# Kernel optimization log

Hardware: AMD Instinct MI355X
Metric: run time of the kernel (lower is better)

## Reference

```python
import jax, jax.numpy as jnp
import numpy as np

D_MODEL = 1024
NUM_HEADS = 16
D_K = D_MODEL // NUM_HEADS
LOCAL_WINDOW = 3
STRIDE = 4


def strided_mask(seq_len):
    # position i attends to j iff j <= i and (i-j <= local_window or (i-j) % stride == 0)
    i = jnp.arange(seq_len)[:, None]
    j = jnp.arange(seq_len)[None, :]
    d = i - j
    return (d >= 0) & ((d <= LOCAL_WINDOW) | (d % STRIDE == 0))


def setup_inputs() -> dict:
    key = jax.random.key(0)
    ks = jax.random.split(key, 11)
    B, S, D = 4, 1024, D_MODEL
    s = 1.0 / np.sqrt(D)
    inp = {
        "Q": jax.random.normal(ks[0], (B, S, D), jnp.float32),
        "K": jax.random.normal(ks[1], (B, S, D), jnp.float32),
        "V": jax.random.normal(ks[2], (B, S, D), jnp.float32),
        "Wq": jax.random.normal(ks[3], (D, D), jnp.float32) * s,
        "bq": jnp.zeros((D,), jnp.float32),
        "Wk": jax.random.normal(ks[4], (D, D), jnp.float32) * s,
        "bk": jnp.zeros((D,), jnp.float32),
        "Wv": jax.random.normal(ks[5], (D, D), jnp.float32) * s,
        "bv": jnp.zeros((D,), jnp.float32),
        "Wo": jax.random.normal(ks[6], (D, D), jnp.float32) * s,
        "bo": jnp.zeros((D,), jnp.float32),
    }
    return inp


def reference(Q, K, V, Wq, bq, Wk, bk, Wv, bv, Wo, bo):
    B, S, D = Q.shape
    H, dk = NUM_HEADS, D_K

    def split(x):  # [B,S,D] -> [B,H,S,dk]
        return x.reshape(B, S, H, dk).transpose(0, 2, 1, 3)

    q = split(Q @ Wq + bq)
    k = split(K @ Wk + bk)
    v = split(V @ Wv + bv)

    scores = jnp.einsum("bhsd,bhtd->bhst", q, k) / jnp.sqrt(
        jnp.asarray(dk, jnp.float32))
    m = strided_mask(S)[None, None]  # [1,1,S,S]
    scores = jnp.where(m, scores, -1e9)
    attn = jax.nn.softmax(scores, axis=-1)
    out = jnp.einsum("bhst,bhtd->bhsd", attn, v)
    out = out.transpose(0, 2, 1, 3).reshape(B, S, D)  # combine heads
    return out @ Wo + bo
```

## Files before the change

kernel.cpp:

```cpp
#include <hip/hip_runtime.h>

typedef _Float16 f16;
typedef __attribute__((ext_vector_type(8))) _Float16 f16x8;
typedef __attribute__((ext_vector_type(4))) _Float16 f16x4;
typedef __attribute__((ext_vector_type(4))) float f32x4;

#define MFMA16(a, b, c) __builtin_amdgcn_mfma_f32_16x16x32_f16((a), (b), (c), 0, 0, 0)

__device__ __forceinline__ void gld_lds16(const void* g, void* l) {
  __builtin_amdgcn_global_load_lds(
      (__attribute__((address_space(1))) void*)const_cast<void*>(g),
      (__attribute__((address_space(3))) void*)l, 16, 0, 0);
}

__device__ __forceinline__ f16x8 ld8(const f16* p) { return *(const f16x8*)p; }

__device__ __forceinline__ f16x8 cvt8(const float4& a, const float4& b) {
  f16x8 h;
  h[0] = (f16)a.x; h[1] = (f16)a.y; h[2] = (f16)a.z; h[3] = (f16)a.w;
  h[4] = (f16)b.x; h[5] = (f16)b.y; h[6] = (f16)b.z; h[7] = (f16)b.w;
  return h;
}

__global__ __launch_bounds__(256) void cvt_wT_kernel(
    const float* __restrict__ Wq, const float* __restrict__ Wk,
    const float* __restrict__ Wv, const float* __restrict__ Wo,
    f16* __restrict__ Tq, f16* __restrict__ Tk, f16* __restrict__ Tv, f16* __restrict__ To) {
  const int z = blockIdx.z;
  const float* W = z == 0 ? Wq : (z == 1 ? Wk : (z == 2 ? Wv : Wo));
  f16* T = z == 0 ? Tq : (z == 1 ? Tk : (z == 2 ? Tv : To));
  __shared__ float tile[64][65];
  const int k0 = blockIdx.x * 64, n0 = blockIdx.y * 64;
  const int tx = threadIdx.x & 63, ty = threadIdx.x >> 6;
#pragma unroll
  for (int rr = 0; rr < 16; ++rr) {
    int r = rr * 4 + ty;
    tile[r][tx] = W[(size_t)(k0 + r) * 1024 + n0 + tx];
  }
  __syncthreads();
#pragma unroll
  for (int rr = 0; rr < 16; ++rr) {
    int nn = rr * 4 + ty;
    T[(size_t)(n0 + nn) * 1024 + k0 + tx] = (f16)tile[tx][nn];
  }
}

__global__ __launch_bounds__(256) void gemm_qkv_kernel(
    const float* __restrict__ Q32, const float* __restrict__ K32, const float* __restrict__ V32,
    const f16* __restrict__ Bq, const f16* __restrict__ Bk, const f16* __restrict__ Bv,
    const float* __restrict__ bq, const float* __restrict__ bk, const float* __restrict__ bv,
    f16* __restrict__ qh, f16* __restrict__ kh, f16* __restrict__ kg,
    f16* __restrict__ vh, f16* __restrict__ vtg) {
  const int z = blockIdx.z;
  const float* A32 = z == 0 ? Q32 : (z == 1 ? K32 : V32);
  const f16* Bt = z == 0 ? Bq : (z == 1 ? Bk : Bv);
  const float* bias = z == 0 ? bq : (z == 1 ? bk : bv);

  __shared__ alignas(16) f16 lA[128 * 32];
  __shared__ alignas(16) f16 lB[128 * 32];

  const int t = threadIdx.x;
  const int w = t >> 6, lane = t & 63, quad = lane >> 4, l15 = lane & 15;
  const int wm = w >> 1, wn = w & 1;
  const int mbase = blockIdx.x * 128;
  const int nbase = blockIdx.y * 128;

  const f32x4 zero4 = {0.f, 0.f, 0.f, 0.f};
  f32x4 acc[4][4];
#pragma unroll
  for (int mi = 0; mi < 4; ++mi)
#pragma unroll
    for (int ni = 0; ni < 4; ++ni) acc[mi][ni] = zero4;

  const int r = t >> 2;
  const int koff = (t & 3) * 8;
  const float* ap0 = A32 + (size_t)(mbase + r) * 1024 + koff;
  const float* ap1 = A32 + (size_t)(mbase + 64 + r) * 1024 + koff;

  float4 pa0 = *(const float4*)(ap0);
  float4 pa1 = *(const float4*)(ap0 + 4);
  float4 pb0 = *(const float4*)(ap1);
  float4 pb1 = *(const float4*)(ap1 + 4);

  for (int k0 = 0; k0 < 1024; k0 += 32) {
    __syncthreads();
    *(f16x8*)((char*)lA + t * 16) = cvt8(pa0, pa1);
    *(f16x8*)((char*)lA + 4096 + t * 16) = cvt8(pb0, pb1);
    gld_lds16(Bt + (size_t)(nbase + r) * 1024 + k0 + koff, (char*)lB + w * 1024);
    gld_lds16(Bt + (size_t)(nbase + 64 + r) * 1024 + k0 + koff, (char*)lB + 4096 + w * 1024);
    if (k0 + 32 < 1024) {
      pa0 = *(const float4*)(ap0 + k0 + 32);
      pa1 = *(const float4*)(ap0 + k0 + 36);
      pb0 = *(const float4*)(ap1 + k0 + 32);
      pb1 = *(const float4*)(ap1 + k0 + 36);
    }
    __syncthreads();

    f16x8 af[4], bf[4];
#pragma unroll
    for (int mi = 0; mi < 4; ++mi)
      af[mi] = ld8(&lA[(wm * 64 + mi * 16 + l15) * 32 + quad * 8]);
#pragma unroll
    for (int ni = 0; ni < 4; ++ni)
      bf[ni] = ld8(&lB[(wn * 64 + ni * 16 + l15) * 32 + quad * 8]);
#pragma unroll
    for (int mi = 0; mi < 4; ++mi)
#pragma unroll
      for (int ni = 0; ni < 4; ++ni)
        acc[mi][ni] = MFMA16(af[mi], bf[ni], acc[mi][ni]);
  }

#pragma unroll
  for (int mi = 0; mi < 4; ++mi) {
#pragma unroll
    for (int ni = 0; ni < 4; ++ni) {
#pragma unroll
      for (int rg = 0; rg < 4; ++rg) {
        const int row = mbase + wm * 64 + mi * 16 + quad * 4 + rg;
        const int col = nbase + wn * 64 + ni * 16 + l15;
        const float v = acc[mi][ni][rg] + bias[col];
        const int bh = (row >> 10) * 16 + (col >> 6);
        const int s = row & 1023, d = col & 63;
        const f16 hv = (f16)v;
        if (z == 0) {
          qh[(size_t)bh * 65536 + s * 64 + d] = hv;
        } else if (z == 1) {
          kh[(size_t)bh * 65536 + s * 64 + d] = hv;
          kg[(((size_t)bh * 4 + (s & 3)) * 256 + (s >> 2)) * 64 + d] = hv;
        } else {
          vh[(size_t)bh * 65536 + s * 64 + d] = hv;
          const int rr = s & 3, n = s >> 2, wi = n & 63;
          vtg[(size_t)bh * 65536 + (size_t)rr * 16384 + (size_t)d * 256 +
              (n & ~63) + ((wi & 15) << 2) + (wi >> 4)] = hv;
        }
      }
    }
  }
}

__global__ __launch_bounds__(256) void gemm_out_kernel(
    const f16* __restrict__ A, const f16* __restrict__ Bt,
    const float* __restrict__ bias, float* __restrict__ Cf) {
  __shared__ alignas(16) f16 lA[64 * 32];
  __shared__ alignas(16) f16 lB[128 * 32];

  const int t = threadIdx.x;
  const int w = t >> 6, lane = t & 63, quad = lane >> 4, l15 = lane & 15;
  const int wm = w >> 1, wn = w & 1;
  const int mbase = blockIdx.x * 64;
  const int nbase = blockIdx.y * 128;

  const f32x4 zero4 = {0.f, 0.f, 0.f, 0.f};
  f32x4 acc[2][4];
#pragma unroll
  for (int mi = 0; mi < 2; ++mi)
#pragma unroll
    for (int ni = 0; ni < 4; ++ni) acc[mi][ni] = zero4;

  const int r = t >> 2;
  const int koff = (t & 3) * 8;

  for (int k0 = 0; k0 < 1024; k0 += 32) {
    __syncthreads();
    gld_lds16(A + (size_t)(mbase + r) * 1024 + k0 + koff, (char*)lA + w * 1024);
    gld_lds16(Bt + (size_t)(nbase + r) * 1024 + k0 + koff, (char*)lB + w * 1024);
    gld_lds16(Bt + (size_t)(nbase + 64 + r) * 1024 + k0 + koff, (char*)lB + 4096 + w * 1024);
    __syncthreads();

    f16x8 af[2], bf[4];
#pragma unroll
    for (int mi = 0; mi < 2; ++mi)
      af[mi] = ld8(&lA[(wm * 32 + mi * 16 + l15) * 32 + quad * 8]);
#pragma unroll
    for (int ni = 0; ni < 4; ++ni)
      bf[ni] = ld8(&lB[(wn * 64 + ni * 16 + l15) * 32 + quad * 8]);
#pragma unroll
    for (int mi = 0; mi < 2; ++mi)
#pragma unroll
      for (int ni = 0; ni < 4; ++ni)
        acc[mi][ni] = MFMA16(af[mi], bf[ni], acc[mi][ni]);
  }

#pragma unroll
  for (int mi = 0; mi < 2; ++mi)
#pragma unroll
    for (int ni = 0; ni < 4; ++ni)
#pragma unroll
      for (int rg = 0; rg < 4; ++rg) {
        const int row = mbase + wm * 32 + mi * 16 + quad * 4 + rg;
        const int col = nbase + wn * 64 + ni * 16 + l15;
        Cf[(size_t)row * 1024 + col] = acc[mi][ni][rg] + bias[col];
      }
}

__global__ __launch_bounds__(256) void attn_far_kernel(
    const f16* __restrict__ qh, const f16* __restrict__ kg,
    const f16* __restrict__ vtg, float* __restrict__ po, float* __restrict__ ml) {
  const int t = threadIdx.x;
  const int w = t >> 6, lane = t & 63, quad = lane >> 4, l15 = lane & 15;
  const int widx = blockIdx.x + 512 * w;
  const int bh = (widx & 255) >> 2, r = widx & 3;
  const int wq = widx >> 8;
  const int m0 = wq * 32;
  const int ntiles = (wq >> 1) + 1;

  __shared__ alignas(16) f16 lp[4][2][16 * 72];

  const f16* qb = qh + (size_t)bh * 65536;
  const f16* kb = kg + ((size_t)bh * 4 + r) * 16384;
  const f16* vb = vtg + (size_t)bh * 65536 + (size_t)r * 16384;
  const float SCL2 = 0.125f * 1.44269504f;

  f16x8 aq[2][2];
#pragma unroll
  for (int mt = 0; mt < 2; ++mt) {
    const int i = 4 * (m0 + mt * 16 + l15) + r;
#pragma unroll
    for (int ko = 0; ko < 2; ++ko)
      aq[mt][ko] = ld8(qb + (size_t)i * 64 + ko * 32 + quad * 8);
  }

  const f32x4 zero4 = {0.f, 0.f, 0.f, 0.f};
  f32x4 o[2][4];
  float mrun[2][4], lrun[2][4];
#pragma unroll
  for (int mt = 0; mt < 2; ++mt)
#pragma unroll
    for (int i = 0; i < 4; ++i) {
      o[mt][i] = zero4; mrun[mt][i] = -1e30f; lrun[mt][i] = 0.f;
    }

  for (int jt = 0; jt < ntiles; ++jt) {
    const int n0 = jt * 64;
    f16x8 bk0[4], bk1[4], bv0[4], bv1[4];
#pragma unroll
    for (int nt = 0; nt < 4; ++nt) {
      const f16* kr = kb + (size_t)(n0 + nt * 16 + l15) * 64;
      bk0[nt] = ld8(kr + quad * 8);
      bk1[nt] = ld8(kr + 32 + quad * 8);
      const f16* vr = vb + (size_t)(nt * 16 + l15) * 256 + n0;
      bv0[nt] = ld8(vr + quad * 8);
      bv1[nt] = ld8(vr + 32 + quad * 8);
    }
    const bool lastt = (jt == ntiles - 1);
#pragma unroll
    for (int mt = 0; mt < 2; ++mt) {
      f32x4 sc[4];
#pragma unroll
      for (int nt = 0; nt < 4; ++nt) {
        f32x4 c = MFMA16(aq[mt][0], bk0[nt], zero4);
        sc[nt] = MFMA16(aq[mt][1], bk1[nt], c);
      }
#pragma unroll
      for (int rg = 0; rg < 4; ++rg) {
        const int m = m0 + mt * 16 + quad * 4 + rg;
        float s[4];
#pragma unroll
        for (int nt = 0; nt < 4; ++nt) {
          float vsc = sc[nt][rg] * SCL2;
          if (lastt) vsc = (n0 + nt * 16 + l15 < m) ? vsc : -3.0e38f;
          s[nt] = vsc;
        }
        float tm = fmaxf(fmaxf(s[0], s[1]), fmaxf(s[2], s[3]));
        tm = fmaxf(tm, __shfl_xor(tm, 1));
        tm = fmaxf(tm, __shfl_xor(tm, 2));
        tm = fmaxf(tm, __shfl_xor(tm, 4));
        tm = fmaxf(tm, __shfl_xor(tm, 8));
        const float mnew = fmaxf(mrun[mt][rg], tm);
        const float alpha = exp2f(mrun[mt][rg] - mnew);
        float p[4], ps = 0.f;
#pragma unroll
        for (int nt = 0; nt < 4; ++nt) { p[nt] = exp2f(s[nt] - mnew); ps += p[nt]; }
        ps += __shfl_xor(ps, 1);
        ps += __shfl_xor(ps, 2);
        ps += __shfl_xor(ps, 4);
        ps += __shfl_xor(ps, 8);
        lrun[mt][rg] = lrun[mt][rg] * alpha + ps;
        mrun[mt][rg] = mnew;
#pragma unroll
        for (int ntv = 0; ntv < 4; ++ntv) o[mt][ntv][rg] *= alpha;
        f16x4 pk;
        pk.x = (f16)p[0]; pk.y = (f16)p[1]; pk.z = (f16)p[2]; pk.w = (f16)p[3];
        *(f16x4*)&lp[w][mt][(quad * 4 + rg) * 72 + l15 * 4] = pk;
      }
    }
#pragma unroll
    for (int mt = 0; mt < 2; ++mt) {
      const f16x8 ap0 = ld8(&lp[w][mt][l15 * 72 + quad * 8]);
      const f16x8 ap1 = ld8(&lp[w][mt][l15 * 72 + 32 + quad * 8]);
#pragma unroll
      for (int ntv = 0; ntv < 4; ++ntv) {
        f32x4 c = MFMA16(ap0, bv0[ntv], o[mt][ntv]);
        o[mt][ntv] = MFMA16(ap1, bv1[ntv], c);
      }
    }
  }

#pragma unroll
  for (int mt = 0; mt < 2; ++mt)
#pragma unroll
    for (int rg = 0; rg < 4; ++rg) {
      const int i = 4 * (m0 + mt * 16 + quad * 4 + rg) + r;
      const size_t idx = (size_t)bh * 1024 + i;
#pragma unroll
      for (int ntv = 0; ntv < 4; ++ntv)
        po[idx * 64 + ntv * 16 + l15] = o[mt][ntv][rg];
      if (l15 == 0) { ml[idx * 2] = mrun[mt][rg]; ml[idx * 2 + 1] = lrun[mt][rg]; }
    }
}

__global__ __launch_bounds__(256) void attn_diag_kernel(
    const f16* __restrict__ qh, const f16* __restrict__ kh, const f16* __restrict__ vh,
    const float* __restrict__ po, const float* __restrict__ ml, f16* __restrict__ ao) {
  const int t = threadIdx.x;
  const int widx = blockIdx.x * 4 + (t >> 6);
  const int l = t & 63;
  const int bh = widx >> 10, i = widx & 1023;
  const float SCL2 = 0.125f * 1.44269504f;

  const float q = (float)qh[(size_t)bh * 65536 + (size_t)i * 64 + l];
  float s[4];
#pragma unroll
  for (int d = 0; d < 4; ++d) {
    const int j = i - d;
    const int jc = j < 0 ? 0 : j;
    float pr = q * (float)kh[(size_t)bh * 65536 + (size_t)jc * 64 + l];
    pr += __shfl_xor(pr, 1);
    pr += __shfl_xor(pr, 2);
    pr += __shfl_xor(pr, 4);
    pr += __shfl_xor(pr, 8);
    pr += __shfl_xor(pr, 16);
    pr += __shfl_xor(pr, 32);
    s[d] = (j >= 0) ? pr * SCL2 : -3.0e38f;
  }
  const float md = fmaxf(fmaxf(s[0], s[1]), fmaxf(s[2], s[3]));
  const size_t idx = (size_t)bh * 1024 + i;
  const float mf = ml[idx * 2], lf = ml[idx * 2 + 1];
  const float M = fmaxf(md, mf);
  float p[4], ld = 0.f;
#pragma unroll
  for (int d = 0; d < 4; ++d) { p[d] = exp2f(s[d] - M); ld += p[d]; }
  float ov = 0.f;
#pragma unroll
  for (int d = 0; d < 4; ++d) {
    const int jc = (i - d) < 0 ? 0 : (i - d);
    ov += p[d] * (float)vh[(size_t)bh * 65536 + (size_t)jc * 64 + l];
  }
  const float fs = exp2f(mf - M);
  const float lt = lf * fs + ld;
  const float of = po[idx * 64 + l];
  const float res = (of * fs + ov) / lt;
  const int b = bh >> 4, h = bh & 15;
  ao[((size_t)(b * 1024 + i)) * 1024 + h * 64 + l] = (f16)res;
}

extern "C" void kernel_launch(void* const* d_in, const int* in_sizes, int n_in,
                              void* d_out, int out_size, void* d_ws, size_t ws_size,
                              hipStream_t stream) {
  const float* Q = (const float*)d_in[0];
  const float* K = (const float*)d_in[1];
  const float* V = (const float*)d_in[2];
  const float* Wq = (const float*)d_in[3];
  const float* bq = (const float*)d_in[4];
  const float* Wk = (const float*)d_in[5];
  const float* bk = (const float*)d_in[6];
  const float* Wv = (const float*)d_in[7];
  const float* bv = (const float*)d_in[8];
  const float* Wo = (const float*)d_in[9];
  const float* bo = (const float*)d_in[10];
  float* out = (float*)d_out;

  char* ws = (char*)d_ws;
  const size_t MB = 1ull << 20;
  f16* TWo = (f16*)(ws + 0 * MB);
  f16* TWq = (f16*)(ws + 2 * MB);
  f16* TWk = (f16*)(ws + 4 * MB);
  f16* TWv = (f16*)(ws + 6 * MB);
  f16* qhb = (f16*)(ws + 8 * MB);
  f16* khb = (f16*)(ws + 16 * MB);
  f16* vhb = (f16*)(ws + 24 * MB);
  f16* vtg = (f16*)(ws + 32 * MB);
  f16* kgb = (f16*)(ws + 40 * MB);
  float* po = (float*)(ws + 48 * MB);
  float* mlb = (float*)(ws + 2 * MB);
  f16* aob = (f16*)(ws + 32 * MB);

  cvt_wT_kernel<<<dim3(16, 16, 4), 256, 0, stream>>>(Wq, Wk, Wv, Wo, TWq, TWk, TWv, TWo);
  gemm_qkv_kernel<<<dim3(32, 8, 3), 256, 0, stream>>>(
      Q, K, V, TWq, TWk, TWv, bq, bk, bv, qhb, khb, kgb, vhb, vtg);
  attn_far_kernel<<<dim3(512), 256, 0, stream>>>(qhb, kgb, vtg, po, mlb);
  attn_diag_kernel<<<dim3(16384), 256, 0, stream>>>(qhb, khb, vhb, po, mlb, aob);
  gemm_out_kernel<<<dim3(64, 8), 256, 0, stream>>>(aob, TWo, bo, out);
}
```

Measured before the change: 249.3 us.

## Pre-convert inputs to fp16, halve GEMM N-tiles, drop redundant K copy

Adds a separate kernel that converts Q/K/V to fp16 so the QKV GEMM can load A tiles with direct global-to-LDS loads instead of converting in registers. It also halves the N tile of both GEMMs to 64, doubling the grid for better CU occupancy. The row-major K copy is removed and the diagonal kernel reads from the grouped K layout instead. The cost is an extra pass over the input activations and more total memory traffic, plus lower per-block reuse of the A tiles.

```diff
diff --git a/kernel.cpp b/kernel.cpp
--- a/kernel.cpp
+++ b/kernel.cpp
@@ -15,11 +15,18 @@
 
 __device__ __forceinline__ f16x8 ld8(const f16* p) { return *(const f16x8*)p; }
 
-__device__ __forceinline__ f16x8 cvt8(const float4& a, const float4& b) {
+__global__ __launch_bounds__(256) void cvt_x_kernel(
+    const float* __restrict__ Q, const float* __restrict__ K, const float* __restrict__ V,
+    f16* __restrict__ oq, f16* __restrict__ ok, f16* __restrict__ ov) {
+  const float* src = blockIdx.z == 0 ? Q : (blockIdx.z == 1 ? K : V);
+  f16* dst = blockIdx.z == 0 ? oq : (blockIdx.z == 1 ? ok : ov);
+  size_t i = ((size_t)blockIdx.x * 256 + threadIdx.x) * 8;
+  float4 a = *(const float4*)(src + i);
+  float4 b = *(const float4*)(src + i + 4);
   f16x8 h;
   h[0] = (f16)a.x; h[1] = (f16)a.y; h[2] = (f16)a.z; h[3] = (f16)a.w;
   h[4] = (f16)b.x; h[5] = (f16)b.y; h[6] = (f16)b.z; h[7] = (f16)b.w;
-  return h;
+  *(f16x8*)(dst + i) = h;
 }
 
 __global__ __launch_bounds__(256) void cvt_wT_kernel(
@@ -46,78 +53,64 @@
 }
 
 __global__ __launch_bounds__(256) void gemm_qkv_kernel(
-    const float* __restrict__ Q32, const float* __restrict__ K32, const float* __restrict__ V32,
+    const f16* __restrict__ Xq, const f16* __restrict__ Xk, const f16* __restrict__ Xv,
     const f16* __restrict__ Bq, const f16* __restrict__ Bk, const f16* __restrict__ Bv,
     const float* __restrict__ bq, const float* __restrict__ bk, const float* __restrict__ bv,
-    f16* __restrict__ qh, f16* __restrict__ kh, f16* __restrict__ kg,
+    f16* __restrict__ qh, f16* __restrict__ kg,
     f16* __restrict__ vh, f16* __restrict__ vtg) {
   const int z = blockIdx.z;
-  const float* A32 = z == 0 ? Q32 : (z == 1 ? K32 : V32);
+  const f16* A = z == 0 ? Xq : (z == 1 ? Xk : Xv);
   const f16* Bt = z == 0 ? Bq : (z == 1 ? Bk : Bv);
   const float* bias = z == 0 ? bq : (z == 1 ? bk : bv);
 
   __shared__ alignas(16) f16 lA[128 * 32];
-  __shared__ alignas(16) f16 lB[128 * 32];
+  __shared__ alignas(16) f16 lB[64 * 32];
 
   const int t = threadIdx.x;
   const int w = t >> 6, lane = t & 63, quad = lane >> 4, l15 = lane & 15;
   const int wm = w >> 1, wn = w & 1;
   const int mbase = blockIdx.x * 128;
-  const int nbase = blockIdx.y * 128;
+  const int nbase = blockIdx.y * 64;
 
   const f32x4 zero4 = {0.f, 0.f, 0.f, 0.f};
-  f32x4 acc[4][4];
+  f32x4 acc[4][2];
 #pragma unroll
   for (int mi = 0; mi < 4; ++mi)
 #pragma unroll
-    for (int ni = 0; ni < 4; ++ni) acc[mi][ni] = zero4;
+    for (int ni = 0; ni < 2; ++ni) acc[mi][ni] = zero4;
 
   const int r = t >> 2;
   const int koff = (t & 3) * 8;
-  const float* ap0 = A32 + (size_t)(mbase + r) * 1024 + koff;
-  const float* ap1 = A32 + (size_t)(mbase + 64 + r) * 1024 + koff;
-
-  float4 pa0 = *(const float4*)(ap0);
-  float4 pa1 = *(const float4*)(ap0 + 4);
-  float4 pb0 = *(const float4*)(ap1);
-  float4 pb1 = *(const float4*)(ap1 + 4);
 
   for (int k0 = 0; k0 < 1024; k0 += 32) {
     __syncthreads();
-    *(f16x8*)((char*)lA + t * 16) = cvt8(pa0, pa1);
-    *(f16x8*)((char*)lA + 4096 + t * 16) = cvt8(pb0, pb1);
+    gld_lds16(A + (size_t)(mbase + r) * 1024 + k0 + koff, (char*)lA + w * 1024);
+    gld_lds16(A + (size_t)(mbase + 64 + r) * 1024 + k0 + koff, (char*)lA + 4096 + w * 1024);
     gld_lds16(Bt + (size_t)(nbase + r) * 1024 + k0 + koff, (char*)lB + w * 1024);
-    gld_lds16(Bt + (size_t)(nbase + 64 + r) * 1024 + k0 + koff, (char*)lB + 4096 + w * 1024);
-    if (k0 + 32 < 1024) {
-      pa0 = *(const float4*)(ap0 + k0 + 32);
-      pa1 = *(const float4*)(ap0 + k0 + 36);
-      pb0 = *(const float4*)(ap1 + k0 + 32);
-      pb1 = *(const float4*)(ap1 + k0 + 36);
-    }
     __syncthreads();
 
-    f16x8 af[4], bf[4];
+    f16x8 af[4], bf[2];
 #pragma unroll
     for (int mi = 0; mi < 4; ++mi)
       af[mi] = ld8(&lA[(wm * 64 + mi * 16 + l15) * 32 + quad * 8]);
 #pragma unroll
-    for (int ni = 0; ni < 4; ++ni)
-      bf[ni] = ld8(&lB[(wn * 64 + ni * 16 + l15) * 32 + quad * 8]);
+    for (int ni = 0; ni < 2; ++ni)
+      bf[ni] = ld8(&lB[(wn * 32 + ni * 16 + l15) * 32 + quad * 8]);
 #pragma unroll
     for (int mi = 0; mi < 4; ++mi)
 #pragma unroll
-      for (int ni = 0; ni < 4; ++ni)
+      for (int ni = 0; ni < 2; ++ni)
         acc[mi][ni] = MFMA16(af[mi], bf[ni], acc[mi][ni]);
   }
 
 #pragma unroll
   for (int mi = 0; mi < 4; ++mi) {
 #pragma unroll
-    for (int ni = 0; ni < 4; ++ni) {
+    for (int ni = 0; ni < 2; ++ni) {
 #pragma unroll
       for (int rg = 0; rg < 4; ++rg) {
         const int row = mbase + wm * 64 + mi * 16 + quad * 4 + rg;
-        const int col = nbase + wn * 64 + ni * 16 + l15;
+        const int col = nbase + wn * 32 + ni * 16 + l15;
         const float v = acc[mi][ni][rg] + bias[col];
         const int bh = (row >> 10) * 16 + (col >> 6);
         const int s = row & 1023, d = col & 63;
@@ -125,7 +118,6 @@
         if (z == 0) {
           qh[(size_t)bh * 65536 + s * 64 + d] = hv;
         } else if (z == 1) {
-          kh[(size_t)bh * 65536 + s * 64 + d] = hv;
           kg[(((size_t)bh * 4 + (s & 3)) * 256 + (s >> 2)) * 64 + d] = hv;
         } else {
           vh[(size_t)bh * 65536 + s * 64 + d] = hv;
@@ -142,20 +134,20 @@
     const f16* __restrict__ A, const f16* __restrict__ Bt,
     const float* __restrict__ bias, float* __restrict__ Cf) {
   __shared__ alignas(16) f16 lA[64 * 32];
-  __shared__ alignas(16) f16 lB[128 * 32];
+  __shared__ alignas(16) f16 lB[64 * 32];
 
   const int t = threadIdx.x;
   const int w = t >> 6, lane = t & 63, quad = lane >> 4, l15 = lane & 15;
   const int wm = w >> 1, wn = w & 1;
   const int mbase = blockIdx.x * 64;
-  const int nbase = blockIdx.y * 128;
+  const int nbase = blockIdx.y * 64;
 
   const f32x4 zero4 = {0.f, 0.f, 0.f, 0.f};
-  f32x4 acc[2][4];
+  f32x4 acc[2][2];
 #pragma unroll
   for (int mi = 0; mi < 2; ++mi)
 #pragma unroll
-    for (int ni = 0; ni < 4; ++ni) acc[mi][ni] = zero4;
+    for (int ni = 0; ni < 2; ++ni) acc[mi][ni] = zero4;
 
   const int r = t >> 2;
   const int koff = (t & 3) * 8;
@@ -164,31 +156,30 @@
     __syncthreads();
     gld_lds16(A + (size_t)(mbase + r) * 1024 + k0 + koff, (char*)lA + w * 1024);
     gld_lds16(Bt + (size_t)(nbase + r) * 1024 + k0 + koff, (char*)lB + w * 1024);
-    gld_lds16(Bt + (size_t)(nbase + 64 + r) * 1024 + k0 + koff, (char*)lB + 4096 + w * 1024);
     __syncthreads();
 
-    f16x8 af[2], bf[4];
+    f16x8 af[2], bf[2];
 #pragma unroll
     for (int mi = 0; mi < 2; ++mi)
       af[mi] = ld8(&lA[(wm * 32 + mi * 16 + l15) * 32 + quad * 8]);
 #pragma unroll
-    for (int ni = 0; ni < 4; ++ni)
-      bf[ni] = ld8(&lB[(wn * 64 + ni * 16 + l15) * 32 + quad * 8]);
+    for (int ni = 0; ni < 2; ++ni)
+      bf[ni] = ld8(&lB[(wn * 32 + ni * 16 + l15) * 32 + quad * 8]);
 #pragma unroll
     for (int mi = 0; mi < 2; ++mi)
 #pragma unroll
-      for (int ni = 0; ni < 4; ++ni)
+      for (int ni = 0; ni < 2; ++ni)
         acc[mi][ni] = MFMA16(af[mi], bf[ni], acc[mi][ni]);
   }
 
 #pragma unroll
   for (int mi = 0; mi < 2; ++mi)
 #pragma unroll
-    for (int ni = 0; ni < 4; ++ni)
+    for (int ni = 0; ni < 2; ++ni)
 #pragma unroll
       for (int rg = 0; rg < 4; ++rg) {
         const int row = mbase + wm * 32 + mi * 16 + quad * 4 + rg;
-        const int col = nbase + wn * 64 + ni * 16 + l15;
+        const int col = nbase + wn * 32 + ni * 16 + l15;
         Cf[(size_t)row * 1024 + col] = acc[mi][ni][rg] + bias[col];
       }
 }
@@ -310,7 +301,7 @@
 }
 
 __global__ __launch_bounds__(256) void attn_diag_kernel(
-    const f16* __restrict__ qh, const f16* __restrict__ kh, const f16* __restrict__ vh,
+    const f16* __restrict__ qh, const f16* __restrict__ kg, const f16* __restrict__ vh,
     const float* __restrict__ po, const float* __restrict__ ml, f16* __restrict__ ao) {
   const int t = threadIdx.x;
   const int widx = blockIdx.x * 4 + (t >> 6);
@@ -324,7 +315,7 @@
   for (int d = 0; d < 4; ++d) {
     const int j = i - d;
     const int jc = j < 0 ? 0 : j;
-    float pr = q * (float)kh[(size_t)bh * 65536 + (size_t)jc * 64 + l];
+    float pr = q * (float)kg[(((size_t)bh * 4 + (jc & 3)) * 256 + (jc >> 2)) * 64 + l];
     pr += __shfl_xor(pr, 1);
     pr += __shfl_xor(pr, 2);
     pr += __shfl_xor(pr, 4);
@@ -376,19 +367,22 @@
   f16* TWq = (f16*)(ws + 2 * MB);
   f16* TWk = (f16*)(ws + 4 * MB);
   f16* TWv = (f16*)(ws + 6 * MB);
-  f16* qhb = (f16*)(ws + 8 * MB);
-  f16* khb = (f16*)(ws + 16 * MB);
-  f16* vhb = (f16*)(ws + 24 * MB);
-  f16* vtg = (f16*)(ws + 32 * MB);
-  f16* kgb = (f16*)(ws + 40 * MB);
-  float* po = (float*)(ws + 48 * MB);
-  float* mlb = (float*)(ws + 2 * MB);
-  f16* aob = (f16*)(ws + 32 * MB);
-
+  f16* Xq  = (f16*)(ws + 8 * MB);
+  f16* Xk  = (f16*)(ws + 16 * MB);
+  f16* Xv  = (f16*)(ws + 24 * MB);
+  f16* qhb = (f16*)(ws + 32 * MB);
+  f16* vhb = (f16*)(ws + 40 * MB);
+  f16* kgb = (f16*)(ws + 48 * MB);
+  f16* vtg = (f16*)(ws + 56 * MB);
+  float* po  = (float*)(ws + 8 * MB);
+  float* mlb = (float*)(ws + 24 * MB);
+  f16* aob   = (f16*)(ws + 56 * MB);
+
+  cvt_x_kernel<<<dim3(2048, 1, 3), 256, 0, stream>>>(Q, K, V, Xq, Xk, Xv);
   cvt_wT_kernel<<<dim3(16, 16, 4), 256, 0, stream>>>(Wq, Wk, Wv, Wo, TWq, TWk, TWv, TWo);
-  gemm_qkv_kernel<<<dim3(32, 8, 3), 256, 0, stream>>>(
-      Q, K, V, TWq, TWk, TWv, bq, bk, bv, qhb, khb, kgb, vhb, vtg);
+  gemm_qkv_kernel<<<dim3(32, 16, 3), 256, 0, stream>>>(
+      Xq, Xk, Xv, TWq, TWk, TWv, bq, bk, bv, qhb, kgb, vhb, vtg);
   attn_far_kernel<<<dim3(512), 256, 0, stream>>>(qhb, kgb, vtg, po, mlb);
-  attn_diag_kernel<<<dim3(16384), 256, 0, stream>>>(qhb, khb, vhb, po, mlb, aob);
-  gemm_out_kernel<<<dim3(64, 8), 256, 0, stream>>>(aob, TWo, bo, out);
-}
+  attn_diag_kernel<<<dim3(16384), 256, 0, stream>>>(qhb, kgb, vhb, po, mlb, aob);
+  gemm_out_kernel<<<dim3(64, 16), 256, 0, stream>>>(aob, TWo, bo, out);
+}
```

Measured after the change: 232.8 us. 1.07x faster.

## Pre-convert activations to fp16 in a fused prep kernel and drop K gather copy

Applied to the files above, without the earlier changes.

A single prep kernel now converts Q/K/V activations to fp16 and transposes and converts the weights, replacing the weight-only conversion kernel. The QKV GEMM then loads A tiles straight into LDS with direct global-to-LDS loads instead of converting fp32 in registers. The strided kg copy of K is removed, and attn_far reads K from kh with strided row indexing. This adds an extra fp16 write and read of the activations but halves the GEMM's A-load bytes and removes one scattered output write.

```diff
diff --git a/kernel.cpp b/kernel.cpp
--- a/kernel.cpp
+++ b/kernel.cpp
@@ -15,44 +15,54 @@
 
 __device__ __forceinline__ f16x8 ld8(const f16* p) { return *(const f16x8*)p; }
 
-__device__ __forceinline__ f16x8 cvt8(const float4& a, const float4& b) {
-  f16x8 h;
-  h[0] = (f16)a.x; h[1] = (f16)a.y; h[2] = (f16)a.z; h[3] = (f16)a.w;
-  h[4] = (f16)b.x; h[5] = (f16)b.y; h[6] = (f16)b.z; h[7] = (f16)b.w;
-  return h;
-}
-
-__global__ __launch_bounds__(256) void cvt_wT_kernel(
+__global__ __launch_bounds__(256) void prep_kernel(
+    const float* __restrict__ Q, const float* __restrict__ K, const float* __restrict__ V,
     const float* __restrict__ Wq, const float* __restrict__ Wk,
     const float* __restrict__ Wv, const float* __restrict__ Wo,
+    f16* __restrict__ Xq, f16* __restrict__ Xk, f16* __restrict__ Xv,
     f16* __restrict__ Tq, f16* __restrict__ Tk, f16* __restrict__ Tv, f16* __restrict__ To) {
-  const int z = blockIdx.z;
-  const float* W = z == 0 ? Wq : (z == 1 ? Wk : (z == 2 ? Wv : Wo));
-  f16* T = z == 0 ? Tq : (z == 1 ? Tk : (z == 2 ? Tv : To));
+  const int bx = blockIdx.x;
   __shared__ float tile[64][65];
-  const int k0 = blockIdx.x * 64, n0 = blockIdx.y * 64;
-  const int tx = threadIdx.x & 63, ty = threadIdx.x >> 6;
-#pragma unroll
-  for (int rr = 0; rr < 16; ++rr) {
-    int r = rr * 4 + ty;
-    tile[r][tx] = W[(size_t)(k0 + r) * 1024 + n0 + tx];
-  }
-  __syncthreads();
-#pragma unroll
-  for (int rr = 0; rr < 16; ++rr) {
-    int nn = rr * 4 + ty;
-    T[(size_t)(n0 + nn) * 1024 + k0 + tx] = (f16)tile[tx][nn];
+  if (bx < 6144) {
+    const int z = bx >> 11, blk = bx & 2047;
+    const float* src = z == 0 ? Q : (z == 1 ? K : V);
+    f16* dst = z == 0 ? Xq : (z == 1 ? Xk : Xv);
+    size_t i = ((size_t)blk * 256 + threadIdx.x) * 8;
+    float4 a = *(const float4*)(src + i);
+    float4 b = *(const float4*)(src + i + 4);
+    f16x8 h;
+    h[0] = (f16)a.x; h[1] = (f16)a.y; h[2] = (f16)a.z; h[3] = (f16)a.w;
+    h[4] = (f16)b.x; h[5] = (f16)b.y; h[6] = (f16)b.z; h[7] = (f16)b.w;
+    *(f16x8*)(dst + i) = h;
+  } else {
+    const int idx = bx - 6144;
+    const int z = idx >> 8, xy = idx & 255;
+    const float* W = z == 0 ? Wq : (z == 1 ? Wk : (z == 2 ? Wv : Wo));
+    f16* T = z == 0 ? Tq : (z == 1 ? Tk : (z == 2 ? Tv : To));
+    const int k0 = (xy & 15) * 64, n0 = (xy >> 4) * 64;
+    const int tx = threadIdx.x & 63, ty = threadIdx.x >> 6;
+#pragma unroll
+    for (int rr = 0; rr < 16; ++rr) {
+      int r = rr * 4 + ty;
+      tile[r][tx] = W[(size_t)(k0 + r) * 1024 + n0 + tx];
+    }
+    __syncthreads();
+#pragma unroll
+    for (int rr = 0; rr < 16; ++rr) {
+      int nn = rr * 4 + ty;
+      T[(size_t)(n0 + nn) * 1024 + k0 + tx] = (f16)tile[tx][nn];
+    }
   }
 }
 
 __global__ __launch_bounds__(256) void gemm_qkv_kernel(
-    const float* __restrict__ Q32, const float* __restrict__ K32, const float* __restrict__ V32,
+    const f16* __restrict__ Xq, const f16* __restrict__ Xk, const f16* __restrict__ Xv,
     const f16* __restrict__ Bq, const f16* __restrict__ Bk, const f16* __restrict__ Bv,
     const float* __restrict__ bq, const float* __restrict__ bk, const float* __restrict__ bv,
-    f16* __restrict__ qh, f16* __restrict__ kh, f16* __restrict__ kg,
+    f16* __restrict__ qh, f16* __restrict__ kh,
     f16* __restrict__ vh, f16* __restrict__ vtg) {
   const int z = blockIdx.z;
-  const float* A32 = z == 0 ? Q32 : (z == 1 ? K32 : V32);
+  const f16* A = z == 0 ? Xq : (z == 1 ? Xk : Xv);
   const f16* Bt = z == 0 ? Bq : (z == 1 ? Bk : Bv);
   const float* bias = z == 0 ? bq : (z == 1 ? bk : bv);
 
@@ -74,26 +84,13 @@
 
   const int r = t >> 2;
   const int koff = (t & 3) * 8;
-  const float* ap0 = A32 + (size_t)(mbase + r) * 1024 + koff;
-  const float* ap1 = A32 + (size_t)(mbase + 64 + r) * 1024 + koff;
-
-  float4 pa0 = *(const float4*)(ap0);
-  float4 pa1 = *(const float4*)(ap0 + 4);
-  float4 pb0 = *(const float4*)(ap1);
-  float4 pb1 = *(const float4*)(ap1 + 4);
 
   for (int k0 = 0; k0 < 1024; k0 += 32) {
     __syncthreads();
-    *(f16x8*)((char*)lA + t * 16) = cvt8(pa0, pa1);
-    *(f16x8*)((char*)lA + 4096 + t * 16) = cvt8(pb0, pb1);
+    gld_lds16(A + (size_t)(mbase + r) * 1024 + k0 + koff, (char*)lA + w * 1024);
+    gld_lds16(A + (size_t)(mbase + 64 + r) * 1024 + k0 + koff, (char*)lA + 4096 + w * 1024);
     gld_lds16(Bt + (size_t)(nbase + r) * 1024 + k0 + koff, (char*)lB + w * 1024);
     gld_lds16(Bt + (size_t)(nbase + 64 + r) * 1024 + k0 + koff, (char*)lB + 4096 + w * 1024);
-    if (k0 + 32 < 1024) {
-      pa0 = *(const float4*)(ap0 + k0 + 32);
-      pa1 = *(const float4*)(ap0 + k0 + 36);
-      pb0 = *(const float4*)(ap1 + k0 + 32);
-      pb1 = *(const float4*)(ap1 + k0 + 36);
-    }
     __syncthreads();
 
     f16x8 af[4], bf[4];
@@ -126,7 +123,6 @@
           qh[(size_t)bh * 65536 + s * 64 + d] = hv;
         } else if (z == 1) {
           kh[(size_t)bh * 65536 + s * 64 + d] = hv;
-          kg[(((size_t)bh * 4 + (s & 3)) * 256 + (s >> 2)) * 64 + d] = hv;
         } else {
           vh[(size_t)bh * 65536 + s * 64 + d] = hv;
           const int rr = s & 3, n = s >> 2, wi = n & 63;
@@ -194,7 +190,7 @@
 }
 
 __global__ __launch_bounds__(256) void attn_far_kernel(
-    const f16* __restrict__ qh, const f16* __restrict__ kg,
+    const f16* __restrict__ qh, const f16* __restrict__ kh,
     const f16* __restrict__ vtg, float* __restrict__ po, float* __restrict__ ml) {
   const int t = threadIdx.x;
   const int w = t >> 6, lane = t & 63, quad = lane >> 4, l15 = lane & 15;
@@ -207,7 +203,7 @@
   __shared__ alignas(16) f16 lp[4][2][16 * 72];
 
   const f16* qb = qh + (size_t)bh * 65536;
-  const f16* kb = kg + ((size_t)bh * 4 + r) * 16384;
+  const f16* kb = kh + (size_t)bh * 65536;
   const f16* vb = vtg + (size_t)bh * 65536 + (size_t)r * 16384;
   const float SCL2 = 0.125f * 1.44269504f;
 
@@ -235,7 +231,7 @@
     f16x8 bk0[4], bk1[4], bv0[4], bv1[4];
 #pragma unroll
     for (int nt = 0; nt < 4; ++nt) {
-      const f16* kr = kb + (size_t)(n0 + nt * 16 + l15) * 64;
+      const f16* kr = kb + (size_t)(4 * (n0 + nt * 16 + l15) + r) * 64;
       bk0[nt] = ld8(kr + quad * 8);
       bk1[nt] = ld8(kr + 32 + quad * 8);
       const f16* vr = vb + (size_t)(nt * 16 + l15) * 256 + n0;
@@ -376,19 +372,22 @@
   f16* TWq = (f16*)(ws + 2 * MB);
   f16* TWk = (f16*)(ws + 4 * MB);
   f16* TWv = (f16*)(ws + 6 * MB);
-  f16* qhb = (f16*)(ws + 8 * MB);
-  f16* khb = (f16*)(ws + 16 * MB);
-  f16* vhb = (f16*)(ws + 24 * MB);
-  f16* vtg = (f16*)(ws + 32 * MB);
-  f16* kgb = (f16*)(ws + 40 * MB);
-  float* po = (float*)(ws + 48 * MB);
-  float* mlb = (float*)(ws + 2 * MB);
-  f16* aob = (f16*)(ws + 32 * MB);
-
-  cvt_wT_kernel<<<dim3(16, 16, 4), 256, 0, stream>>>(Wq, Wk, Wv, Wo, TWq, TWk, TWv, TWo);
+  f16* Xq  = (f16*)(ws + 8 * MB);
+  f16* Xk  = (f16*)(ws + 16 * MB);
+  f16* Xv  = (f16*)(ws + 24 * MB);
+  f16* qhb = (f16*)(ws + 32 * MB);
+  f16* khb = (f16*)(ws + 40 * MB);
+  f16* vhb = (f16*)(ws + 48 * MB);
+  f16* vtg = (f16*)(ws + 56 * MB);
+  float* po  = (float*)(ws + 8 * MB);
+  float* mlb = (float*)(ws + 24 * MB);
+  f16* aob   = (f16*)(ws + 56 * MB);
+
+  prep_kernel<<<dim3(7168), 256, 0, stream>>>(
+      Q, K, V, Wq, Wk, Wv, Wo, Xq, Xk, Xv, TWq, TWk, TWv, TWo);
   gemm_qkv_kernel<<<dim3(32, 8, 3), 256, 0, stream>>>(
-      Q, K, V, TWq, TWk, TWv, bq, bk, bv, qhb, khb, kgb, vhb, vtg);
-  attn_far_kernel<<<dim3(512), 256, 0, stream>>>(qhb, kgb, vtg, po, mlb);
+      Xq, Xk, Xv, TWq, TWk, TWv, bq, bk, bv, qhb, khb, vhb, vtg);
+  attn_far_kernel<<<dim3(512), 256, 0, stream>>>(qhb, khb, vtg, po, mlb);
   attn_diag_kernel<<<dim3(16384), 256, 0, stream>>>(qhb, khb, vhb, po, mlb, aob);
   gemm_out_kernel<<<dim3(64, 8), 256, 0, stream>>>(aob, TWo, bo, out);
 }
```

After: 238.9 us. -4.2%, faster.
